# Kernel optimization log

Hardware: AMD Instinct MI355X
Metric: run time of the kernel (lower is better)

## Reference

```python
import jax, jax.numpy as jnp
import numpy as np

N_NODES = 100000
N_EDGES = 1600000
IN_CH = 64
HEADS = 8
OUT_CH = 16
NEG_SLOPE = 0.2  # PyG GATConv default


def setup_inputs() -> dict:
    key = jax.random.key(0)
    ks = jax.random.split(key, 6)
    x = jax.random.normal(ks[0], (N_NODES, IN_CH), dtype=jnp.float32)
    edge_index = jax.random.randint(ks[1], (2, N_EDGES), 0, N_NODES, dtype=jnp.int32)
    # learned parameters (PyG GATConv: shared lin for src/dst, att vectors, bias for concat output)
    W = jax.random.normal(ks[2], (HEADS * OUT_CH, IN_CH), dtype=jnp.float32) / np.sqrt(IN_CH)
    att_src = jax.random.normal(ks[3], (HEADS, OUT_CH), dtype=jnp.float32) / np.sqrt(OUT_CH)
    att_dst = jax.random.normal(ks[4], (HEADS, OUT_CH), dtype=jnp.float32) / np.sqrt(OUT_CH)
    bias = jax.random.normal(ks[5], (HEADS * OUT_CH,), dtype=jnp.float32) * 0.01
    return {"x": x, "edge_index": edge_index, "W": W,
            "att_src": att_src, "att_dst": att_dst, "bias": bias}


def reference(x, edge_index, W, att_src, att_dst, bias):
    n = x.shape[0]
    # linear projection -> [N, H, C]
    h = (x @ W.T).reshape(n, HEADS, OUT_CH)
    # per-node halves of the attention logit
    a_src = jnp.einsum('nhc,hc->nh', h, att_src)  # [N, H]
    a_dst = jnp.einsum('nhc,hc->nh', h, att_dst)  # [N, H]
    # add self loops (PyG default add_self_loops=True)
    loops = jnp.arange(n, dtype=edge_index.dtype)
    src = jnp.concatenate([edge_index[0], loops])
    dst = jnp.concatenate([edge_index[1], loops])
    # edge attention: leaky_relu then segment-softmax over incoming edges of dst
    e = jax.nn.leaky_relu(a_src[src] + a_dst[dst], NEG_SLOPE)  # [E+N, H]
    e_max = jax.ops.segment_max(e, dst, num_segments=n)
    e = jnp.exp(e - e_max[dst])
    denom = jax.ops.segment_sum(e, dst, num_segments=n)
    alpha = e / (denom[dst] + 1e-16)  # [E+N, H]
    # weighted scatter-add aggregation
    msg = h[src] * alpha[:, :, None]  # [E+N, H, C]
    out = jax.ops.segment_sum(msg, dst, num_segments=n).reshape(n, HEADS * OUT_CH)
    out = out + bias
    # unlinear: act='relu', norm=None
    return jax.nn.relu(out)
```

## Files before the change

kernel.cpp:

```cpp
#include <hip/hip_runtime.h>

#define N_NODESC 100000
#define N_EDGESC 1600000
#define IN_CHC 64
#define HEADSC 8
#define OUT_CHC 16
#define HCC 128
#define E_TOTC (N_EDGESC + N_NODESC)
#define SCAN_NB 391
#define PROJ_NB 782
#define POS_NB 831

__device__ __forceinline__ float lrelu(float v) {
    return v < 0.f ? 0.2f * v : v;
}
__device__ __forceinline__ unsigned short f2bf(float f) {
    unsigned u = __float_as_uint(f);
    unsigned r = ((u >> 16) & 1u) + 0x7fffu;
    return (unsigned short)((u + r) >> 16);
}

__launch_bounds__(256, 2)
__global__ void proj_pos_kernel(const float* __restrict__ x, const float* __restrict__ W,
                                const float* __restrict__ att_src, const float* __restrict__ att_dst,
                                unsigned short* __restrict__ h16,
                                float* __restrict__ a_src, float* __restrict__ a_dst,
                                const int* __restrict__ ei, int* __restrict__ deg,
                                int* __restrict__ posb) {
    const int t = threadIdx.x;

    if (blockIdx.x >= PROJ_NB) {
        const int e0 = (blockIdx.x - PROJ_NB) * 2048 + t;
#pragma unroll
        for (int j = 0; j < 8; ++j) {
            int e = e0 + 256 * j;
            if (e < E_TOTC) {
                int d = (e < N_EDGESC) ? ei[N_EDGESC + e] : (e - N_EDGESC);
                posb[e] = atomicAdd(&deg[d], 1);
            }
        }
        return;
    }

    __shared__ float xs[128][68];
    __shared__ float ws[64][132];
    const int row0 = blockIdx.x * 128;

    const float4* W4 = (const float4*)W;
#pragma unroll
    for (int j = 0; j < 8; ++j) {
        int q = t + 256 * j;
        float4 v = W4[q];
        int c = q >> 4;
        int k0 = (q & 15) * 4;
        ws[k0 + 0][c] = v.x; ws[k0 + 1][c] = v.y;
        ws[k0 + 2][c] = v.z; ws[k0 + 3][c] = v.w;
    }

#pragma unroll
    for (int j = 0; j < 8; ++j) {
        int f = (t + 256 * j) * 4;
        int r = f >> 6, k = f & 63;
        int gr = row0 + r;
        if (gr >= N_NODESC) gr = N_NODESC - 1;
        float4 v = *(const float4*)&x[(size_t)gr * IN_CHC + k];
        *(float4*)&xs[r][k] = v;
    }
    __syncthreads();

    const int rg = t & 15;
    const int cg = t >> 4;
    float acc[8][8];
#pragma unroll
    for (int i = 0; i < 8; ++i)
#pragma unroll
        for (int j = 0; j < 8; ++j) acc[i][j] = 0.f;

#pragma unroll 4
    for (int k = 0; k < 64; ++k) {
        float xv[8];
#pragma unroll
        for (int i = 0; i < 8; ++i) xv[i] = xs[rg + 16 * i][k];
        float4 w0 = *(const float4*)&ws[k][4 * cg];
        float4 w1 = *(const float4*)&ws[k][64 + 4 * cg];
#pragma unroll
        for (int i = 0; i < 8; ++i) {
            acc[i][0] += xv[i] * w0.x; acc[i][1] += xv[i] * w0.y;
            acc[i][2] += xv[i] * w0.z; acc[i][3] += xv[i] * w0.w;
            acc[i][4] += xv[i] * w1.x; acc[i][5] += xv[i] * w1.y;
            acc[i][6] += xv[i] * w1.z; acc[i][7] += xv[i] * w1.w;
        }
    }

    const int cg4 = cg & 3;
    const int hA = cg >> 2, hB = (cg >> 2) + 4;
    float4 sA = *(const float4*)&att_src[hA * 16 + 4 * cg4];
    float4 dA = *(const float4*)&att_dst[hA * 16 + 4 * cg4];
    float4 sB = *(const float4*)&att_src[hB * 16 + 4 * cg4];
    float4 dB = *(const float4*)&att_dst[hB * 16 + 4 * cg4];

#pragma unroll
    for (int i = 0; i < 8; ++i) {
        int gr = row0 + rg + 16 * i;
        float asA = acc[i][0] * sA.x + acc[i][1] * sA.y + acc[i][2] * sA.z + acc[i][3] * sA.w;
        float adA = acc[i][0] * dA.x + acc[i][1] * dA.y + acc[i][2] * dA.z + acc[i][3] * dA.w;
        float asB = acc[i][4] * sB.x + acc[i][5] * sB.y + acc[i][6] * sB.z + acc[i][7] * sB.w;
        float adB = acc[i][4] * dB.x + acc[i][5] * dB.y + acc[i][6] * dB.z + acc[i][7] * dB.w;
        asA += __shfl_xor(asA, 16); asA += __shfl_xor(asA, 32);
        adA += __shfl_xor(adA, 16); adA += __shfl_xor(adA, 32);
        asB += __shfl_xor(asB, 16); asB += __shfl_xor(asB, 32);
        adB += __shfl_xor(adB, 16); adB += __shfl_xor(adB, 32);
        if (gr < N_NODESC) {
            ushort4 p0, p1;
            p0.x = f2bf(acc[i][0]); p0.y = f2bf(acc[i][1]); p0.z = f2bf(acc[i][2]); p0.w = f2bf(acc[i][3]);
            p1.x = f2bf(acc[i][4]); p1.y = f2bf(acc[i][5]); p1.z = f2bf(acc[i][6]); p1.w = f2bf(acc[i][7]);
            *(ushort4*)&h16[(size_t)gr * HCC + 4 * cg] = p0;
            *(ushort4*)&h16[(size_t)gr * HCC + 64 + 4 * cg] = p1;
            if (cg4 == 0) {
                a_src[(size_t)gr * 8 + hA] = asA;
                a_dst[(size_t)gr * 8 + hA] = adA;
                a_src[(size_t)gr * 8 + hB] = asB;
                a_dst[(size_t)gr * 8 + hB] = adB;
            }
        }
    }
}

__global__ void scan1_kernel(const int* __restrict__ deg, int* __restrict__ bsum) {
    __shared__ int lds[256];
    int i = blockIdx.x * 256 + threadIdx.x;
    lds[threadIdx.x] = (i < N_NODESC) ? deg[i] : 0;
    __syncthreads();
    for (int off = 128; off > 0; off >>= 1) {
        if (threadIdx.x < off) lds[threadIdx.x] += lds[threadIdx.x + off];
        __syncthreads();
    }
    if (threadIdx.x == 0) bsum[blockIdx.x] = lds[0];
}

__global__ void scan2_kernel(int* __restrict__ bsum) {
    __shared__ int lds[512];
    int t = threadIdx.x;
    lds[t] = (t < SCAN_NB) ? bsum[t] : 0;
    __syncthreads();
    for (int off = 1; off < 512; off <<= 1) {
        int u = 0;
        if (t >= off) u = lds[t - off];
        __syncthreads();
        if (t >= off) lds[t] += u;
        __syncthreads();
    }
    if (t < SCAN_NB) bsum[t] = (t == 0) ? 0 : lds[t - 1];
}

__global__ void scan3_kernel(const int* __restrict__ deg, const int* __restrict__ bsum,
                             int* __restrict__ rowptr) {
    __shared__ int lds[256];
    int t = threadIdx.x;
    int i = blockIdx.x * 256 + t;
    int v = (i < N_NODESC) ? deg[i] : 0;
    lds[t] = v;
    __syncthreads();
    for (int off = 1; off < 256; off <<= 1) {
        int u = 0;
        if (t >= off) u = lds[t - off];
        __syncthreads();
        if (t >= off) lds[t] += u;
        __syncthreads();
    }
    int excl = bsum[blockIdx.x] + lds[t] - v;
    if (i < N_NODESC) rowptr[i] = excl;
    if (i == 0) rowptr[N_NODESC] = E_TOTC;
}

__global__ void scatter_kernel(const int* __restrict__ ei, const int* __restrict__ rowptr,
                               const int* __restrict__ posb, int* __restrict__ colsrc) {
    int e = blockIdx.x * 256 + threadIdx.x;
    if (e >= E_TOTC) return;
    int s, d;
    if (e < N_EDGESC) { s = ei[e]; d = ei[N_EDGESC + e]; }
    else              { s = d = e - N_EDGESC; }
    colsrc[rowptr[d] + posb[e]] = s;
}

__launch_bounds__(256, 8)
__global__ void agg_csr_kernel(const int* __restrict__ rowptr, const int* __restrict__ colsrc,
                               const float* __restrict__ a_src, const float* __restrict__ a_dst,
                               const unsigned* __restrict__ h32,
                               const float* __restrict__ bias, float* __restrict__ out) {
    const int t = threadIdx.x;
    const int L = t & 63;
    const int n = blockIdx.x * 4 + (t >> 6);
    const int hd = L >> 3;
    const int eL = L & 7;

    const int beg = rowptr[n], end = rowptr[n + 1];
    const float ad = a_dst[n * 8 + hd];

    float m = -1e30f, den = 0.f;
    float acc[16];
#pragma unroll
    for (int j = 0; j < 16; ++j) acc[j] = 0.f;

    bool vld = eL < (end - beg);
    int s = vld ? colsrc[beg + eL] : 0;
    float av = vld ? a_src[s * 8 + hd] : 0.f;

    for (int p0 = beg; p0 < end; p0 += 8) {
        uint4 ha = make_uint4(0, 0, 0, 0), hb = make_uint4(0, 0, 0, 0);
        if (vld) {
            const uint4* hp = (const uint4*)(h32 + (size_t)s * 64 + hd * 8);
            ha = hp[0];
            hb = hp[1];
        }
        bool vld2 = (p0 + 8 + eL) < end;
        int s2 = vld2 ? colsrc[p0 + 8 + eL] : 0;
        float av2 = vld2 ? a_src[s2 * 8 + hd] : 0.f;

        float l = vld ? lrelu(av + ad) : -1e30f;
        float mx = l;
        mx = fmaxf(mx, __shfl_xor(mx, 1));
        mx = fmaxf(mx, __shfl_xor(mx, 2));
        mx = fmaxf(mx, __shfl_xor(mx, 4));
        const float mn = fmaxf(m, mx);
        const float sc = __expf(m - mn);
        float p = vld ? __expf(l - mn) : 0.f;
        float cs = p;
        cs += __shfl_xor(cs, 1);
        cs += __shfl_xor(cs, 2);
        cs += __shfl_xor(cs, 4);
        den = den * sc + cs;
        m = mn;
#pragma unroll
        for (int j = 0; j < 16; ++j) acc[j] *= sc;

        acc[0]  = fmaf(p, __uint_as_float(ha.x << 16),        acc[0]);
        acc[1]  = fmaf(p, __uint_as_float(ha.x & 0xffff0000u), acc[1]);
        acc[2]  = fmaf(p, __uint_as_float(ha.y << 16),        acc[2]);
        acc[3]  = fmaf(p, __uint_as_float(ha.y & 0xffff0000u), acc[3]);
        acc[4]  = fmaf(p, __uint_as_float(ha.z << 16),        acc[4]);
        acc[5]  = fmaf(p, __uint_as_float(ha.z & 0xffff0000u), acc[5]);
        acc[6]  = fmaf(p, __uint_as_float(ha.w << 16),        acc[6]);
        acc[7]  = fmaf(p, __uint_as_float(ha.w & 0xffff0000u), acc[7]);
        acc[8]  = fmaf(p, __uint_as_float(hb.x << 16),        acc[8]);
        acc[9]  = fmaf(p, __uint_as_float(hb.x & 0xffff0000u), acc[9]);
        acc[10] = fmaf(p, __uint_as_float(hb.y << 16),        acc[10]);
        acc[11] = fmaf(p, __uint_as_float(hb.y & 0xffff0000u), acc[11]);
        acc[12] = fmaf(p, __uint_as_float(hb.z << 16),        acc[12]);
        acc[13] = fmaf(p, __uint_as_float(hb.z & 0xffff0000u), acc[13]);
        acc[14] = fmaf(p, __uint_as_float(hb.w << 16),        acc[14]);
        acc[15] = fmaf(p, __uint_as_float(hb.w & 0xffff0000u), acc[15]);

        s = s2; av = av2; vld = vld2;
    }

#pragma unroll
    for (int j = 0; j < 16; ++j) {
        acc[j] += __shfl_xor(acc[j], 1);
        acc[j] += __shfl_xor(acc[j], 2);
        acc[j] += __shfl_xor(acc[j], 4);
    }
    const float inv = 1.f / (den + 1e-16f);
    float ox = acc[0], oy = acc[1];
#pragma unroll
    for (int j = 1; j < 8; ++j) {
        ox = (eL == j) ? acc[2 * j]     : ox;
        oy = (eL == j) ? acc[2 * j + 1] : oy;
    }
    const float2 b = ((const float2*)bias)[L];
    float2 o;
    o.x = fmaxf(ox * inv + b.x, 0.f);
    o.y = fmaxf(oy * inv + b.y, 0.f);
    ((float2*)out)[(size_t)n * 64 + L] = o;
}

extern "C" void kernel_launch(void* const* d_in, const int* in_sizes, int n_in,
                              void* d_out, int out_size, void* d_ws, size_t ws_size,
                              hipStream_t stream) {
    const float* x       = (const float*)d_in[0];
    const int*   ei      = (const int*)d_in[1];
    const float* W       = (const float*)d_in[2];
    const float* att_src = (const float*)d_in[3];
    const float* att_dst = (const float*)d_in[4];
    const float* bias    = (const float*)d_in[5];
    float* out = (float*)d_out;

    float* ws    = (float*)d_ws;
    unsigned short* h16 = (unsigned short*)ws;
    float* a_src = ws + 6400000;
    float* a_dst = a_src + 800000;
    int* deg     = (int*)(a_dst + 800000);
    int* rowptr  = deg + 100000;
    int* bsum    = rowptr + 100001;
    int* posb    = bsum + 512;
    int* colsrc  = posb + 1700000;

    hipMemsetAsync(deg, 0, 100000 * sizeof(int), stream);

    proj_pos_kernel<<<PROJ_NB + POS_NB, 256, 0, stream>>>(x, W, att_src, att_dst,
                                                          h16, a_src, a_dst,
                                                          ei, deg, posb);
    scan1_kernel<<<SCAN_NB, 256, 0, stream>>>(deg, bsum);
    scan2_kernel<<<1, 512, 0, stream>>>(bsum);
    scan3_kernel<<<SCAN_NB, 256, 0, stream>>>(deg, bsum, rowptr);
    scatter_kernel<<<(E_TOTC + 255) / 256, 256, 0, stream>>>(ei, rowptr, posb, colsrc);

    agg_csr_kernel<<<N_NODESC / 4, 256, 0, stream>>>(rowptr, colsrc, a_src, a_dst,
                                                     (const unsigned*)h16, bias, out);
}
```

Measured before the change: 219.7 us.

## Use MFMA bf16 for projection and drop online-max softmax in aggregation

The projection GEMM is replaced by per-wave MFMA 16x16x32 bf16 instructions that load x and W directly from global memory and convert them to bf16, removing the LDS tiling. The aggregation kernel drops the running-max rescaling of the segment softmax and accumulates exp(leaky_relu) directly. It reduces the denominator only once at the end, which removes per-chunk shuffles and accumulator rescales. In exchange, exp may overflow for large logits, and the projection inputs lose precision to bf16.

```diff
diff --git a/kernel.cpp b/kernel.cpp
--- a/kernel.cpp
+++ b/kernel.cpp
@@ -2,25 +2,31 @@
 
 #define N_NODESC 100000
 #define N_EDGESC 1600000
-#define IN_CHC 64
-#define HEADSC 8
-#define OUT_CHC 16
 #define HCC 128
 #define E_TOTC (N_EDGESC + N_NODESC)
 #define SCAN_NB 391
-#define PROJ_NB 782
+#define PROJ_NB 1563
 #define POS_NB 831
 
-__device__ __forceinline__ float lrelu(float v) {
-    return v < 0.f ? 0.2f * v : v;
-}
+using short8 = __attribute__((ext_vector_type(8))) short;
+using f32x4  = __attribute__((ext_vector_type(4))) float;
+
+__device__ __forceinline__ float lrelu(float v) { return fmaxf(v, 0.2f * v); }
 __device__ __forceinline__ unsigned short f2bf(float f) {
     unsigned u = __float_as_uint(f);
     unsigned r = ((u >> 16) & 1u) + 0x7fffu;
     return (unsigned short)((u + r) >> 16);
 }
-
-__launch_bounds__(256, 2)
+__device__ __forceinline__ short8 pack8(float4 a, float4 b) {
+    short8 v;
+    v[0] = (short)f2bf(a.x); v[1] = (short)f2bf(a.y);
+    v[2] = (short)f2bf(a.z); v[3] = (short)f2bf(a.w);
+    v[4] = (short)f2bf(b.x); v[5] = (short)f2bf(b.y);
+    v[6] = (short)f2bf(b.z); v[7] = (short)f2bf(b.w);
+    return v;
+}
+
+__launch_bounds__(256, 4)
 __global__ void proj_pos_kernel(const float* __restrict__ x, const float* __restrict__ W,
                                 const float* __restrict__ att_src, const float* __restrict__ att_dst,
                                 unsigned short* __restrict__ h16,
@@ -42,85 +48,50 @@
         return;
     }
 
-    __shared__ float xs[128][68];
-    __shared__ float ws[64][132];
-    const int row0 = blockIdx.x * 128;
-
-    const float4* W4 = (const float4*)W;
-#pragma unroll
-    for (int j = 0; j < 8; ++j) {
-        int q = t + 256 * j;
-        float4 v = W4[q];
-        int c = q >> 4;
-        int k0 = (q & 15) * 4;
-        ws[k0 + 0][c] = v.x; ws[k0 + 1][c] = v.y;
-        ws[k0 + 2][c] = v.z; ws[k0 + 3][c] = v.w;
-    }
-
-#pragma unroll
-    for (int j = 0; j < 8; ++j) {
-        int f = (t + 256 * j) * 4;
-        int r = f >> 6, k = f & 63;
-        int gr = row0 + r;
-        if (gr >= N_NODESC) gr = N_NODESC - 1;
-        float4 v = *(const float4*)&x[(size_t)gr * IN_CHC + k];
-        *(float4*)&xs[r][k] = v;
-    }
-    __syncthreads();
-
-    const int rg = t & 15;
-    const int cg = t >> 4;
-    float acc[8][8];
-#pragma unroll
-    for (int i = 0; i < 8; ++i)
-#pragma unroll
-        for (int j = 0; j < 8; ++j) acc[i][j] = 0.f;
-
-#pragma unroll 4
-    for (int k = 0; k < 64; ++k) {
-        float xv[8];
-#pragma unroll
-        for (int i = 0; i < 8; ++i) xv[i] = xs[rg + 16 * i][k];
-        float4 w0 = *(const float4*)&ws[k][4 * cg];
-        float4 w1 = *(const float4*)&ws[k][64 + 4 * cg];
-#pragma unroll
-        for (int i = 0; i < 8; ++i) {
-            acc[i][0] += xv[i] * w0.x; acc[i][1] += xv[i] * w0.y;
-            acc[i][2] += xv[i] * w0.z; acc[i][3] += xv[i] * w0.w;
-            acc[i][4] += xv[i] * w1.x; acc[i][5] += xv[i] * w1.y;
-            acc[i][6] += xv[i] * w1.z; acc[i][7] += xv[i] * w1.w;
+    const int l  = t & 63;
+    const int lc = l & 15;
+    const int lg = l >> 4;
+    const int row0 = blockIdx.x * 64 + (t >> 6) * 16;
+    const int rA = min(row0 + lc, N_NODESC - 1);
+
+    f32x4 acc[8];
+#pragma unroll
+    for (int i = 0; i < 8; ++i) acc[i] = (f32x4){0.f, 0.f, 0.f, 0.f};
+
+#pragma unroll
+    for (int s = 0; s < 2; ++s) {
+        const float4* xp = (const float4*)(x + (size_t)rA * 64 + s * 32 + lg * 8);
+        float4 x0 = xp[0], x1 = xp[1];
+        short8 af = pack8(x0, x1);
+#pragma unroll
+        for (int t2 = 0; t2 < 8; ++t2) {
+            const float4* wp = (const float4*)(W + (size_t)(t2 * 16 + lc) * 64 + s * 32 + lg * 8);
+            float4 w0 = wp[0], w1 = wp[1];
+            short8 bf = pack8(w0, w1);
+            acc[t2] = __builtin_amdgcn_mfma_f32_16x16x32_bf16(af, bf, acc[t2], 0, 0, 0);
         }
     }
 
-    const int cg4 = cg & 3;
-    const int hA = cg >> 2, hB = (cg >> 2) + 4;
-    float4 sA = *(const float4*)&att_src[hA * 16 + 4 * cg4];
-    float4 dA = *(const float4*)&att_dst[hA * 16 + 4 * cg4];
-    float4 sB = *(const float4*)&att_src[hB * 16 + 4 * cg4];
-    float4 dB = *(const float4*)&att_dst[hB * 16 + 4 * cg4];
-
-#pragma unroll
-    for (int i = 0; i < 8; ++i) {
-        int gr = row0 + rg + 16 * i;
-        float asA = acc[i][0] * sA.x + acc[i][1] * sA.y + acc[i][2] * sA.z + acc[i][3] * sA.w;
-        float adA = acc[i][0] * dA.x + acc[i][1] * dA.y + acc[i][2] * dA.z + acc[i][3] * dA.w;
-        float asB = acc[i][4] * sB.x + acc[i][5] * sB.y + acc[i][6] * sB.z + acc[i][7] * sB.w;
-        float adB = acc[i][4] * dB.x + acc[i][5] * dB.y + acc[i][6] * dB.z + acc[i][7] * dB.w;
-        asA += __shfl_xor(asA, 16); asA += __shfl_xor(asA, 32);
-        adA += __shfl_xor(adA, 16); adA += __shfl_xor(adA, 32);
-        asB += __shfl_xor(asB, 16); asB += __shfl_xor(asB, 32);
-        adB += __shfl_xor(adB, 16); adB += __shfl_xor(adB, 32);
-        if (gr < N_NODESC) {
-            ushort4 p0, p1;
-            p0.x = f2bf(acc[i][0]); p0.y = f2bf(acc[i][1]); p0.z = f2bf(acc[i][2]); p0.w = f2bf(acc[i][3]);
-            p1.x = f2bf(acc[i][4]); p1.y = f2bf(acc[i][5]); p1.z = f2bf(acc[i][6]); p1.w = f2bf(acc[i][7]);
-            *(ushort4*)&h16[(size_t)gr * HCC + 4 * cg] = p0;
-            *(ushort4*)&h16[(size_t)gr * HCC + 64 + 4 * cg] = p1;
-            if (cg4 == 0) {
-                a_src[(size_t)gr * 8 + hA] = asA;
-                a_dst[(size_t)gr * 8 + hA] = adA;
-                a_src[(size_t)gr * 8 + hB] = asB;
-                a_dst[(size_t)gr * 8 + hB] = adB;
+#pragma unroll
+    for (int hd = 0; hd < 8; ++hd) {
+        const float as_ = att_src[hd * 16 + lc];
+        const float ad_ = att_dst[hd * 16 + lc];
+#pragma unroll
+        for (int j = 0; j < 4; ++j) {
+            const int grow = row0 + lg * 4 + j;
+            const float hv = acc[hd][j];
+            float ts = hv * as_;
+            float td = hv * ad_;
+            ts += __shfl_xor(ts, 1); ts += __shfl_xor(ts, 2);
+            ts += __shfl_xor(ts, 4); ts += __shfl_xor(ts, 8);
+            td += __shfl_xor(td, 1); td += __shfl_xor(td, 2);
+            td += __shfl_xor(td, 4); td += __shfl_xor(td, 8);
+            if (grow < N_NODESC) {
+                h16[(size_t)grow * HCC + hd * 16 + lc] = f2bf(hv);
+                if (lc == 0) {
+                    a_src[(size_t)grow * 8 + hd] = ts;
+                    a_dst[(size_t)grow * 8 + hd] = td;
+                }
             }
         }
     }
@@ -197,63 +168,48 @@
     const int beg = rowptr[n], end = rowptr[n + 1];
     const float ad = a_dst[n * 8 + hd];
 
-    float m = -1e30f, den = 0.f;
+    float den = 0.f;
     float acc[16];
 #pragma unroll
     for (int j = 0; j < 16; ++j) acc[j] = 0.f;
 
-    bool vld = eL < (end - beg);
-    int s = vld ? colsrc[beg + eL] : 0;
+    int p = beg + eL;
+    bool vld = p < end;
+    int s = vld ? colsrc[p] : 0;
     float av = vld ? a_src[s * 8 + hd] : 0.f;
 
-    for (int p0 = beg; p0 < end; p0 += 8) {
-        uint4 ha = make_uint4(0, 0, 0, 0), hb = make_uint4(0, 0, 0, 0);
-        if (vld) {
-            const uint4* hp = (const uint4*)(h32 + (size_t)s * 64 + hd * 8);
-            ha = hp[0];
-            hb = hp[1];
-        }
-        bool vld2 = (p0 + 8 + eL) < end;
-        int s2 = vld2 ? colsrc[p0 + 8 + eL] : 0;
-        float av2 = vld2 ? a_src[s2 * 8 + hd] : 0.f;
-
-        float l = vld ? lrelu(av + ad) : -1e30f;
-        float mx = l;
-        mx = fmaxf(mx, __shfl_xor(mx, 1));
-        mx = fmaxf(mx, __shfl_xor(mx, 2));
-        mx = fmaxf(mx, __shfl_xor(mx, 4));
-        const float mn = fmaxf(m, mx);
-        const float sc = __expf(m - mn);
-        float p = vld ? __expf(l - mn) : 0.f;
-        float cs = p;
-        cs += __shfl_xor(cs, 1);
-        cs += __shfl_xor(cs, 2);
-        cs += __shfl_xor(cs, 4);
-        den = den * sc + cs;
-        m = mn;
-#pragma unroll
-        for (int j = 0; j < 16; ++j) acc[j] *= sc;
-
-        acc[0]  = fmaf(p, __uint_as_float(ha.x << 16),        acc[0]);
-        acc[1]  = fmaf(p, __uint_as_float(ha.x & 0xffff0000u), acc[1]);
-        acc[2]  = fmaf(p, __uint_as_float(ha.y << 16),        acc[2]);
-        acc[3]  = fmaf(p, __uint_as_float(ha.y & 0xffff0000u), acc[3]);
-        acc[4]  = fmaf(p, __uint_as_float(ha.z << 16),        acc[4]);
-        acc[5]  = fmaf(p, __uint_as_float(ha.z & 0xffff0000u), acc[5]);
-        acc[6]  = fmaf(p, __uint_as_float(ha.w << 16),        acc[6]);
-        acc[7]  = fmaf(p, __uint_as_float(ha.w & 0xffff0000u), acc[7]);
-        acc[8]  = fmaf(p, __uint_as_float(hb.x << 16),        acc[8]);
-        acc[9]  = fmaf(p, __uint_as_float(hb.x & 0xffff0000u), acc[9]);
-        acc[10] = fmaf(p, __uint_as_float(hb.y << 16),        acc[10]);
-        acc[11] = fmaf(p, __uint_as_float(hb.y & 0xffff0000u), acc[11]);
-        acc[12] = fmaf(p, __uint_as_float(hb.z << 16),        acc[12]);
-        acc[13] = fmaf(p, __uint_as_float(hb.z & 0xffff0000u), acc[13]);
-        acc[14] = fmaf(p, __uint_as_float(hb.w << 16),        acc[14]);
-        acc[15] = fmaf(p, __uint_as_float(hb.w & 0xffff0000u), acc[15]);
-
-        s = s2; av = av2; vld = vld2;
-    }
-
+    while (vld) {
+        const uint4* hp = (const uint4*)(h32 + (size_t)s * 64 + hd * 8);
+        const uint4 ha = hp[0];
+        const uint4 hb = hp[1];
+        const int p2 = p + 8;
+        const bool v2 = p2 < end;
+        const int s2 = v2 ? colsrc[p2] : 0;
+        const float av2 = v2 ? a_src[s2 * 8 + hd] : 0.f;
+
+        const float pr = __expf(lrelu(av + ad));
+        den += pr;
+        acc[0]  = fmaf(pr, __uint_as_float(ha.x << 16),         acc[0]);
+        acc[1]  = fmaf(pr, __uint_as_float(ha.x & 0xffff0000u), acc[1]);
+        acc[2]  = fmaf(pr, __uint_as_float(ha.y << 16),         acc[2]);
+        acc[3]  = fmaf(pr, __uint_as_float(ha.y & 0xffff0000u), acc[3]);
+        acc[4]  = fmaf(pr, __uint_as_float(ha.z << 16),         acc[4]);
+        acc[5]  = fmaf(pr, __uint_as_float(ha.z & 0xffff0000u), acc[5]);
+        acc[6]  = fmaf(pr, __uint_as_float(ha.w << 16),         acc[6]);
+        acc[7]  = fmaf(pr, __uint_as_float(ha.w & 0xffff0000u), acc[7]);
+        acc[8]  = fmaf(pr, __uint_as_float(hb.x << 16),         acc[8]);
+        acc[9]  = fmaf(pr, __uint_as_float(hb.x & 0xffff0000u), acc[9]);
+        acc[10] = fmaf(pr, __uint_as_float(hb.y << 16),         acc[10]);
+        acc[11] = fmaf(pr, __uint_as_float(hb.y & 0xffff0000u), acc[11]);
+        acc[12] = fmaf(pr, __uint_as_float(hb.z << 16),         acc[12]);
+        acc[13] = fmaf(pr, __uint_as_float(hb.z & 0xffff0000u), acc[13]);
+        acc[14] = fmaf(pr, __uint_as_float(hb.w << 16),         acc[14]);
+        acc[15] = fmaf(pr, __uint_as_float(hb.w & 0xffff0000u), acc[15]);
+
+        p = p2; s = s2; av = av2; vld = v2;
+    }
+
+    den += __shfl_xor(den, 1); den += __shfl_xor(den, 2); den += __shfl_xor(den, 4);
 #pragma unroll
     for (int j = 0; j < 16; ++j) {
         acc[j] += __shfl_xor(acc[j], 1);
```

Measured after the change: 226.0 us. 1.03x slower.
